# Optimization experiments

Hardware: AMD Instinct MI355X
Metric: run time of the kernel (lower is better)

## Reference

```python
import jax, jax.numpy as jnp
import numpy as np

N_DRUG = 20000
N_PROT = 30000
N = N_DRUG + N_PROT
F_DRUG = 128
F_PROT = 256
H = 64          # hidden_channels
OUT = 1         # out_channels
E = 1_600_000
L = 200_000
LAYERS = 3


def _lin_init(key, fan_in, fan_out):
    return jax.random.normal(key, (fan_in, fan_out), jnp.float32) / np.sqrt(fan_in)


def setup_inputs() -> dict:
    key = jax.random.key(0)
    ks = jax.random.split(key, 10)
    x_drug = jax.random.normal(ks[0], (N_DRUG, F_DRUG), jnp.float32)
    x_protein = jax.random.normal(ks[1], (N_PROT, F_PROT), jnp.float32)
    edge_index = jax.random.randint(ks[2], (2, E), 0, N, dtype=jnp.int64)
    edge_label_src = jax.random.randint(ks[3], (L,), 0, N_DRUG, dtype=jnp.int64)
    # protein label indices point into the concatenated [drug; protein] tensor
    edge_label_dst = jax.random.randint(ks[4], (L,), 0, N_PROT, dtype=jnp.int64) + N_DRUG
    W_drug = _lin_init(ks[5], F_DRUG, H)
    b_drug = jnp.zeros((H,), jnp.float32)
    W_prot = _lin_init(ks[6], F_PROT, H)
    b_prot = jnp.zeros((H,), jnp.float32)
    conv_W = jax.random.normal(ks[7], (LAYERS, H, H), jnp.float32) / np.sqrt(H)
    conv_b = jnp.zeros((LAYERS, H), jnp.float32)
    lin_W = _lin_init(ks[8], H, OUT)
    lin_b = jnp.zeros((OUT,), jnp.float32)
    return {
        "x_drug": x_drug, "x_protein": x_protein,
        "W_drug": W_drug, "b_drug": b_drug,
        "W_prot": W_prot, "b_prot": b_prot,
        "conv_W": conv_W, "conv_b": conv_b,
        "lin_W": lin_W, "lin_b": lin_b,
        "edge_index": edge_index,
        "edge_label_src": edge_label_src,
        "edge_label_dst": edge_label_dst,
    }


def reference(x_drug, x_protein, W_drug, b_drug, W_prot, b_prot,
              conv_W, conv_b, lin_W, lin_b,
              edge_index, edge_label_src, edge_label_dst):
    # type-specific input projections + relu
    hd = jax.nn.relu(x_drug @ W_drug + b_drug)
    hp = jax.nn.relu(x_protein @ W_prot + b_prot)
    x = jnp.concatenate([hd, hp], axis=0)  # [N, H]

    src, dst = edge_index[0], edge_index[1]
    # GCN normalization with self-loops: deg counts in-edges (by dst) + 1
    deg = jax.ops.segment_sum(jnp.ones_like(src, dtype=x.dtype), dst, num_segments=N) + 1.0
    dis = jax.lax.rsqrt(deg)               # deg >= 1 always
    edge_norm = (dis[src] * dis[dst])[:, None]   # [E, 1]
    self_norm = (dis * dis)[:, None]             # [N, 1]

    for l in range(LAYERS):
        xw = x @ conv_W[l]                                   # [N, H] dense GEMM
        agg = jax.ops.segment_sum(xw[src] * edge_norm, dst, num_segments=N)
        x = jax.nn.relu(agg + xw * self_norm + conv_b[l])

    # edge scoring head: gather endpoints, linear to 1, multiply, sigmoid
    sd = (x[edge_label_src] @ lin_W + lin_b)[:, 0]  # [L]
    sp = (x[edge_label_dst] @ lin_W + lin_b)[:, 0]  # [L]
    return jax.nn.sigmoid(sd * sp)
```

## Files before the change

kernel.cpp:

```cpp
#include <hip/hip_runtime.h>
#include <hip/hip_fp16.h>
#include <math.h>

#define N_DRUG 20000
#define N_PROT 30000
#define NN (N_DRUG + N_PROT)
#define F_DRUG 128
#define F_PROT 256
#define H 64
#define NE 1600000
#define NL 200000

#define NB_PROJD ((N_DRUG + 127) / 128)
#define NB_PROJP ((N_PROT + 127) / 128)
#define NB_CONV  ((NN + 255) / 256)
#define NB_ROW4  ((NN + 3) / 4)
#define NBK1 256
#define CH   ((NE + NBK1 - 1) / NBK1)
#define NB_BKT ((NN + 255) / 256)

typedef _Float16 h8 __attribute__((ext_vector_type(8)));
typedef _Float16 h4 __attribute__((ext_vector_type(4)));
typedef float f32x4 __attribute__((ext_vector_type(4)));

#define MFMA16(a, b, c) __builtin_amdgcn_mfma_f32_16x16x32_f16((a), (b), (c), 0, 0, 0)

__global__ __launch_bounds__(256) void k_wprep(
    const float* __restrict__ Wd, const float* __restrict__ Wp,
    const float* __restrict__ cw,
    _Float16* __restrict__ wdt, _Float16* __restrict__ wpt,
    _Float16* __restrict__ cwt) {
    int i = blockIdx.x * 256 + threadIdx.x;
    if (i < 64 * F_DRUG) {
        int c = i / F_DRUG, k = i % F_DRUG;
        wdt[i] = (_Float16)Wd[k * H + c];
    }
    if (i < 64 * F_PROT) {
        int c = i / F_PROT, k = i % F_PROT;
        wpt[i] = (_Float16)Wp[k * H + c];
    }
    if (i < 3 * 64 * 64) {
        int l = i >> 12, r = i & 4095;
        int c = r >> 6, k = r & 63;
        cwt[i] = (_Float16)cw[(l << 12) + k * H + c];
    }
}

template <int F>
__device__ __forceinline__ void proj_direct(
    const float* __restrict__ X, const _Float16* __restrict__ Wt,
    const float* __restrict__ bias, __half* __restrict__ out,
    int rows, int row_off, int bid) {
    int l = threadIdx.x & 63, wvi = threadIdx.x >> 6;
    int lr = l & 15, lq = l >> 4;
    int r0 = bid * 128 + wvi * 32;
    f32x4 acc[2][4];
    #pragma unroll
    for (int rt = 0; rt < 2; ++rt)
        #pragma unroll
        for (int n = 0; n < 4; ++n) acc[rt][n] = (f32x4){0.f, 0.f, 0.f, 0.f};

    for (int k0 = 0; k0 < F; k0 += 64) {
        h8 af[4][2];
        #pragma unroll
        for (int n = 0; n < 4; ++n)
            #pragma unroll
            for (int kk = 0; kk < 2; ++kk)
                af[n][kk] = *(const h8*)&Wt[(size_t)(n * 16 + lr) * F + k0 + kk * 32 + lq * 8];
        #pragma unroll
        for (int rt = 0; rt < 2; ++rt) {
            int r = r0 + rt * 16 + lr;
            int rc = (r < rows) ? r : (rows - 1);
            h8 bf[2];
            #pragma unroll
            for (int kk = 0; kk < 2; ++kk) {
                const float* xp = X + (size_t)rc * F + k0 + kk * 32 + lq * 8;
                float4 a = *(const float4*)xp;
                float4 b = *(const float4*)(xp + 4);
                h8 t;
                t[0] = (_Float16)a.x; t[1] = (_Float16)a.y;
                t[2] = (_Float16)a.z; t[3] = (_Float16)a.w;
                t[4] = (_Float16)b.x; t[5] = (_Float16)b.y;
                t[6] = (_Float16)b.z; t[7] = (_Float16)b.w;
                bf[kk] = t;
            }
            #pragma unroll
            for (int n = 0; n < 4; ++n) {
                acc[rt][n] = MFMA16(af[n][0], bf[0], acc[rt][n]);
                acc[rt][n] = MFMA16(af[n][1], bf[1], acc[rt][n]);
            }
        }
    }
    #pragma unroll
    for (int rt = 0; rt < 2; ++rt) {
        int r = r0 + rt * 16 + lr;
        if (r < rows) {
            #pragma unroll
            for (int n = 0; n < 4; ++n) {
                int c = n * 16 + lq * 4;
                float4 bv = *(const float4*)&bias[c];
                h4 hv;
                hv[0] = (_Float16)fmaxf(acc[rt][n][0] + bv.x, 0.f);
                hv[1] = (_Float16)fmaxf(acc[rt][n][1] + bv.y, 0.f);
                hv[2] = (_Float16)fmaxf(acc[rt][n][2] + bv.z, 0.f);
                hv[3] = (_Float16)fmaxf(acc[rt][n][3] + bv.w, 0.f);
                *(h4*)((_Float16*)out + (size_t)(row_off + r) * H + c) = hv;
            }
        }
    }
}

__device__ __forceinline__ void conv_direct(
    const __half* __restrict__ xin, const _Float16* __restrict__ Wt,
    __half* __restrict__ xout, int bid) {
    int l = threadIdx.x & 63, wvi = threadIdx.x >> 6;
    int lr = l & 15, lq = l >> 4;
    const _Float16* xh = (const _Float16*)xin;
    h8 af[4][2];
    #pragma unroll
    for (int n = 0; n < 4; ++n)
        #pragma unroll
        for (int kk = 0; kk < 2; ++kk)
            af[n][kk] = *(const h8*)&Wt[(size_t)(n * 16 + lr) * 64 + kk * 32 + lq * 8];
    int r0 = bid * 256 + wvi * 64;
    #pragma unroll
    for (int rt = 0; rt < 4; ++rt) {
        int r = r0 + rt * 16 + lr;
        int rc = (r < NN) ? r : (NN - 1);
        h8 bf0 = *(const h8*)&xh[(size_t)rc * H + lq * 8];
        h8 bf1 = *(const h8*)&xh[(size_t)rc * H + 32 + lq * 8];
        f32x4 a[4];
        #pragma unroll
        for (int n = 0; n < 4; ++n) {
            a[n] = (f32x4){0.f, 0.f, 0.f, 0.f};
            a[n] = MFMA16(af[n][0], bf0, a[n]);
            a[n] = MFMA16(af[n][1], bf1, a[n]);
        }
        if (r < NN) {
            #pragma unroll
            for (int n = 0; n < 4; ++n) {
                int c = n * 16 + lq * 4;
                h4 hv;
                hv[0] = (_Float16)a[n][0]; hv[1] = (_Float16)a[n][1];
                hv[2] = (_Float16)a[n][2]; hv[3] = (_Float16)a[n][3];
                *(h4*)((_Float16*)xout + (size_t)r * H + c) = hv;
            }
        }
    }
}

__global__ __launch_bounds__(256) void k_front(
    const float* __restrict__ xd, const _Float16* __restrict__ wdt, const float* __restrict__ bd,
    const float* __restrict__ xp, const _Float16* __restrict__ wpt, const float* __restrict__ bp,
    const int* __restrict__ ei, unsigned* __restrict__ bhist, __half* __restrict__ xbuf) {
    __shared__ unsigned lh[256];
    int bid = blockIdx.x;
    if (bid < NB_PROJD) {
        proj_direct<F_DRUG>(xd, wdt, bd, xbuf, N_DRUG, 0, bid);
    } else if (bid < NB_PROJD + NB_PROJP) {
        proj_direct<F_PROT>(xp, wpt, bp, xbuf, N_PROT, N_DRUG, bid - NB_PROJD);
    } else {
        int blk = bid - NB_PROJD - NB_PROJP;
        int t = threadIdx.x;
        lh[t] = 0;
        __syncthreads();
        int eb = blk * CH, ee = min(NE, eb + CH);
        for (int e = eb + t; e < ee; e += 256)
            atomicAdd(&lh[((unsigned)ei[NE + e]) >> 8], 1u);
        __syncthreads();
        bhist[(size_t)t * NBK1 + blk] = lh[t];
    }
}

__global__ __launch_bounds__(256) void kA(const unsigned* __restrict__ bhist,
                                          unsigned* __restrict__ rsum) {
    __shared__ unsigned s[256];
    int j = blockIdx.x, t = threadIdx.x;
    s[t] = bhist[(size_t)j * NBK1 + t];
    __syncthreads();
    for (int off = 128; off; off >>= 1) {
        if (t < off) s[t] += s[t + off];
        __syncthreads();
    }
    if (t == 0) rsum[j] = s[0];
}

__global__ __launch_bounds__(256) void kB(const unsigned* __restrict__ rsum,
                                          unsigned* __restrict__ rbase) {
    __shared__ unsigned s[256];
    int t = threadIdx.x;
    unsigned c = rsum[t];
    s[t] = c;
    __syncthreads();
    for (int off = 1; off < 256; off <<= 1) {
        unsigned v = s[t]; unsigned u = (t >= off) ? s[t - off] : 0;
        __syncthreads(); s[t] = v + u; __syncthreads();
    }
    rbase[t] = s[t] - c;
    if (t == 255) rbase[256] = s[255];
}

__global__ __launch_bounds__(256) void kC(unsigned* __restrict__ bhist,
                                          const unsigned* __restrict__ rbase) {
    __shared__ unsigned s[256];
    int j = blockIdx.x, t = threadIdx.x;
    unsigned c = bhist[(size_t)j * NBK1 + t];
    s[t] = c;
    __syncthreads();
    for (int off = 1; off < 256; off <<= 1) {
        unsigned v = s[t]; unsigned u = (t >= off) ? s[t - off] : 0;
        __syncthreads(); s[t] = v + u; __syncthreads();
    }
    bhist[(size_t)j * NBK1 + t] = rbase[j] + s[t] - c;
}

__global__ __launch_bounds__(256) void k_part(
    const int* __restrict__ ei, const unsigned* __restrict__ base,
    unsigned* __restrict__ tmp) {
    __shared__ unsigned lcur[256];
    int bid = blockIdx.x;
    int c = ((bid & 7) << 5) | (bid >> 3);
    int t = threadIdx.x;
    lcur[t] = base[(size_t)t * NBK1 + c];
    __syncthreads();
    int eb = c * CH, ee = min(NE, eb + CH);
    for (int e = eb + t; e < ee; e += 256) {
        unsigned s = (unsigned)ei[e];
        unsigned d = (unsigned)ei[NE + e];
        unsigned pos = atomicAdd(&lcur[d >> 8], 1u);
        tmp[pos] = ((d & 255u) << 16) | s;
    }
}

__global__ __launch_bounds__(256) void k_csrconv(
    const unsigned* __restrict__ tmp, const unsigned* __restrict__ rbase,
    int* __restrict__ rp, float* __restrict__ dis, unsigned short* __restrict__ csr,
    const __half* __restrict__ xbuf, const _Float16* __restrict__ cwt,
    __half* __restrict__ xwh) {
    __shared__ unsigned lbin[256], lofs[256], lcur[256];
    int bid = blockIdx.x;
    if (bid >= NB_BKT) {
        conv_direct(xbuf, cwt, xwh, bid - NB_BKT);
        return;
    }
    int b = bid, t = threadIdx.x;
    unsigned nb0 = rbase[b], nb1 = rbase[b + 1];
    lbin[t] = 0;
    __syncthreads();
    for (unsigned i = nb0 + t; i < nb1; i += 256)
        atomicAdd(&lbin[tmp[i] >> 16], 1u);
    __syncthreads();
    unsigned c = lbin[t];
    lofs[t] = c;
    __syncthreads();
    for (int off = 1; off < 256; off <<= 1) {
        unsigned v = lofs[t]; unsigned u = (t >= off) ? lofs[t - off] : 0;
        __syncthreads(); lofs[t] = v + u; __syncthreads();
    }
    unsigned r = nb0 + lofs[t] - c;
    int node = b * 256 + t;
    if (node < NN) {
        rp[node] = (int)r;
        dis[node] = rsqrtf((float)c + 1.0f);
    }
    lcur[t] = r;
    __syncthreads();
    for (unsigned i = nb0 + t; i < nb1; i += 256) {
        unsigned rec = tmp[i];
        unsigned pos = atomicAdd(&lcur[rec >> 16], 1u);
        csr[pos] = (unsigned short)(rec & 0xffffu);
    }
    if (b == 0 && t == 0) rp[NN] = NE;
}

__global__ __launch_bounds__(256) void k_conv(
    const __half* __restrict__ X, const _Float16* __restrict__ Wt, __half* __restrict__ out) {
    conv_direct(X, Wt, out, blockIdx.x);
}

template <bool FIRST, bool LAST>
__global__ __launch_bounds__(256) void k_spmm(
    const int* __restrict__ rp, const unsigned short* __restrict__ csr,
    unsigned* __restrict__ pack, const float* __restrict__ dis,
    const __half* __restrict__ xw,
    const float* __restrict__ bias, __half* __restrict__ xout,
    const float* __restrict__ lw, const float* __restrict__ lb,
    float* __restrict__ y) {
    int lane = threadIdx.x & 63;
    int d = blockIdx.x * 4 + (threadIdx.x >> 6);
    if (d >= NN) return;
    int q = lane >> 4, g = lane & 15;
    int beg = rp[d], end = rp[d + 1];
    float dd = dis[d];
    const _Float16* xh = (const _Float16*)xw;
    float ax = 0.f, ay = 0.f, az = 0.f, aw = 0.f;

    int n = end - beg; if (n > 64) n = 64;
    unsigned rv = 0;
    if (lane < n) {
        if (FIRST) {
            int s = csr[beg + lane];
            float w0 = dis[s] * dd;
            rv = (unsigned)s | ((unsigned)__half_as_ushort(__float2half(w0)) << 16);
            pack[beg + lane] = rv;
        } else rv = pack[beg + lane];
    }
    for (int b0 = beg; b0 < end; ) {
        int nb = b0 + 64;
        int n2 = end - nb; if (n2 > 64) n2 = 64;
        unsigned rv2 = 0;
        if (n2 > 0 && lane < n2) {
            if (FIRST) {
                int s = csr[nb + lane];
                float w0 = dis[s] * dd;
                rv2 = (unsigned)s | ((unsigned)__half_as_ushort(__float2half(w0)) << 16);
                pack[nb + lane] = rv2;
            } else rv2 = pack[nb + lane];
        }
        int nsteps = (n + 3) >> 2;
        for (int j0 = 0; j0 < nsteps; j0 += 8) {
            int m = nsteps - j0; if (m > 8) m = 8;
            h4 xv[8]; float wv[8];
            #pragma unroll
            for (int k = 0; k < 8; ++k) {
                if (k < m) {
                    unsigned r = __shfl(rv, (j0 + k) * 4 + q);
                    wv[k] = __half2float(__ushort_as_half((unsigned short)(r >> 16)));
                    xv[k] = *(const h4*)&xh[((r & 0xffffu) << 6) + (g << 2)];
                }
            }
            #pragma unroll
            for (int k = 0; k < 8; ++k) {
                if (k < m) {
                    ax += wv[k] * (float)xv[k][0];
                    ay += wv[k] * (float)xv[k][1];
                    az += wv[k] * (float)xv[k][2];
                    aw += wv[k] * (float)xv[k][3];
                }
            }
        }
        b0 = nb; n = n2; rv = rv2;
    }
    ax += __shfl_xor(ax, 16); ay += __shfl_xor(ay, 16);
    az += __shfl_xor(az, 16); aw += __shfl_xor(aw, 16);
    ax += __shfl_xor(ax, 32); ay += __shfl_xor(ay, 32);
    az += __shfl_xor(az, 32); aw += __shfl_xor(aw, 32);

    float sn = dd * dd;
    h4 xs = *(const h4*)&xh[((unsigned)d << 6) + (g << 2)];
    float4 bv = *(const float4*)&bias[g << 2];
    float vx = fmaxf(ax + sn * (float)xs[0] + bv.x, 0.f);
    float vy = fmaxf(ay + sn * (float)xs[1] + bv.y, 0.f);
    float vz = fmaxf(az + sn * (float)xs[2] + bv.z, 0.f);
    float vw = fmaxf(aw + sn * (float)xs[3] + bv.w, 0.f);
    if (LAST) {
        float4 lv = *(const float4*)&lw[g << 2];
        float t = vx * lv.x + vy * lv.y + vz * lv.z + vw * lv.w;
        #pragma unroll
        for (int off = 8; off; off >>= 1) t += __shfl_xor(t, off);
        if (lane == 0) y[d] = t + lb[0];
    } else if (q == 0) {
        h4 hv;
        hv[0] = (_Float16)vx; hv[1] = (_Float16)vy;
        hv[2] = (_Float16)vz; hv[3] = (_Float16)vw;
        *(h4*)((_Float16*)xout + ((size_t)d << 6) + (g << 2)) = hv;
    }
}

__global__ void k_out(const float* __restrict__ y, const int* __restrict__ ls,
                      const int* __restrict__ ld, float* __restrict__ out) {
    int e = blockIdx.x * blockDim.x + threadIdx.x;
    if (e < NL) {
        float z = y[ls[e]] * y[ld[e]];
        out[e] = 1.f / (1.f + __expf(-z));
    }
}

static inline size_t up256(size_t x) { return (x + 255) & ~(size_t)255; }

extern "C" void kernel_launch(void* const* d_in, const int* in_sizes, int n_in,
                              void* d_out, int out_size, void* d_ws, size_t ws_size,
                              hipStream_t stream) {
    const float* x_drug = (const float*)d_in[0];
    const float* x_prot = (const float*)d_in[1];
    const float* W_drug = (const float*)d_in[2];
    const float* b_drug = (const float*)d_in[3];
    const float* W_prot = (const float*)d_in[4];
    const float* b_prot = (const float*)d_in[5];
    const float* conv_W = (const float*)d_in[6];
    const float* conv_b = (const float*)d_in[7];
    const float* lin_W  = (const float*)d_in[8];
    const float* lin_b  = (const float*)d_in[9];
    const int*   ei     = (const int*)d_in[10];
    const int*   lsrc   = (const int*)d_in[11];
    const int*   ldst   = (const int*)d_in[12];
    float* out = (float*)d_out;

    char* w = (char*)d_ws;
    size_t off = 0;
    unsigned* bhist = (unsigned*)(w + off); off = up256(off + (size_t)256 * NBK1 * 4);
    unsigned* rsum  = (unsigned*)(w + off); off = up256(off + 256 * 4);
    unsigned* rbase = (unsigned*)(w + off); off = up256(off + 257 * 4);
    unsigned* tmp   = (unsigned*)(w + off); off = up256(off + (size_t)NE * 4);
    unsigned short* csr = (unsigned short*)(w + off); off = up256(off + (size_t)NE * 2);
    unsigned* pack  = (unsigned*)(w + off); off = up256(off + (size_t)NE * 4);
    int*    rp   = (int*)(w + off);    off = up256(off + (size_t)(NN + 1) * 4);
    float*  dis  = (float*)(w + off);  off = up256(off + (size_t)NN * 4);
    __half* xbuf = (__half*)(w + off); off = up256(off + (size_t)NN * H * 2);
    __half* xwh  = (__half*)(w + off); off = up256(off + (size_t)NN * H * 2);
    float*  y    = (float*)(w + off);  off = up256(off + (size_t)NN * 4);
    _Float16* wdt = (_Float16*)(w + off); off = up256(off + (size_t)64 * F_DRUG * 2);
    _Float16* wpt = (_Float16*)(w + off); off = up256(off + (size_t)64 * F_PROT * 2);
    _Float16* cwt = (_Float16*)(w + off); off = up256(off + (size_t)3 * 64 * 64 * 2);

    k_wprep<<<64, 256, 0, stream>>>(W_drug, W_prot, conv_W, wdt, wpt, cwt);

    k_front<<<NB_PROJD + NB_PROJP + NBK1, 256, 0, stream>>>(
        x_drug, wdt, b_drug, x_prot, wpt, b_prot, ei, bhist, xbuf);

    kA<<<256, 256, 0, stream>>>(bhist, rsum);
    kB<<<1, 256, 0, stream>>>(rsum, rbase);
    kC<<<256, 256, 0, stream>>>(bhist, rbase);

    k_part<<<NBK1, 256, 0, stream>>>(ei, bhist, tmp);

    k_csrconv<<<NB_BKT + NB_CONV, 256, 0, stream>>>(
        tmp, rbase, rp, dis, csr, xbuf, cwt, xwh);

    k_spmm<true, false><<<NB_ROW4, 256, 0, stream>>>(
        rp, csr, pack, dis, xwh, conv_b, xbuf, nullptr, nullptr, nullptr);
    k_conv<<<NB_CONV, 256, 0, stream>>>(xbuf, cwt + 4096, xwh);
    k_spmm<false, false><<<NB_ROW4, 256, 0, stream>>>(
        rp, csr, pack, dis, xwh, conv_b + H, xbuf, nullptr, nullptr, nullptr);
    k_conv<<<NB_CONV, 256, 0, stream>>>(xbuf, cwt + 8192, xwh);
    k_spmm<false, true><<<NB_ROW4, 256, 0, stream>>>(
        rp, csr, pack, dis, xwh, conv_b + 2 * H, nullptr, lin_W, lin_b, y);

    k_out<<<(NL + 255) / 256, 256, 0, stream>>>(y, lsrc, ldst, out);
}
```

Measured before the change: 206.2 us.

## Split hidden features into two 32-wide halves and run SpMM per half

Stores activations as two separate 32-column fp16 planes and runs each sparse aggregation twice, once per half, so each gathered row is 64 bytes and each pass's working set is half as large for better cache hit rates. The pack array is reread with nontemporal loads in the later passes. It doubles the SpMM launches and the CSR/pack traversal. The final linear head is split into two partial sums that the output kernel adds together.

```diff
diff --git a/kernel.cpp b/kernel.cpp
--- a/kernel.cpp
+++ b/kernel.cpp
@@ -49,7 +49,8 @@
 template <int F>
 __device__ __forceinline__ void proj_direct(
     const float* __restrict__ X, const _Float16* __restrict__ Wt,
-    const float* __restrict__ bias, __half* __restrict__ out,
+    const float* __restrict__ bias,
+    _Float16* __restrict__ xlo, _Float16* __restrict__ xhi,
     int rows, int row_off, int bid) {
     int l = threadIdx.x & 63, wvi = threadIdx.x >> 6;
     int lr = l & 15, lq = l >> 4;
@@ -104,18 +105,21 @@
                 hv[1] = (_Float16)fmaxf(acc[rt][n][1] + bv.y, 0.f);
                 hv[2] = (_Float16)fmaxf(acc[rt][n][2] + bv.z, 0.f);
                 hv[3] = (_Float16)fmaxf(acc[rt][n][3] + bv.w, 0.f);
-                *(h4*)((_Float16*)out + (size_t)(row_off + r) * H + c) = hv;
+                _Float16* dst = (n < 2)
+                    ? (xlo + (size_t)(row_off + r) * 32 + c)
+                    : (xhi + (size_t)(row_off + r) * 32 + (c - 32));
+                *(h4*)dst = hv;
             }
         }
     }
 }
 
 __device__ __forceinline__ void conv_direct(
-    const __half* __restrict__ xin, const _Float16* __restrict__ Wt,
-    __half* __restrict__ xout, int bid) {
+    const _Float16* __restrict__ xlo, const _Float16* __restrict__ xhi,
+    const _Float16* __restrict__ Wt,
+    _Float16* __restrict__ olo, _Float16* __restrict__ ohi, int bid) {
     int l = threadIdx.x & 63, wvi = threadIdx.x >> 6;
     int lr = l & 15, lq = l >> 4;
-    const _Float16* xh = (const _Float16*)xin;
     h8 af[4][2];
     #pragma unroll
     for (int n = 0; n < 4; ++n)
@@ -127,8 +131,8 @@
     for (int rt = 0; rt < 4; ++rt) {
         int r = r0 + rt * 16 + lr;
         int rc = (r < NN) ? r : (NN - 1);
-        h8 bf0 = *(const h8*)&xh[(size_t)rc * H + lq * 8];
-        h8 bf1 = *(const h8*)&xh[(size_t)rc * H + 32 + lq * 8];
+        h8 bf0 = *(const h8*)&xlo[(size_t)rc * 32 + lq * 8];
+        h8 bf1 = *(const h8*)&xhi[(size_t)rc * 32 + lq * 8];
         f32x4 a[4];
         #pragma unroll
         for (int n = 0; n < 4; ++n) {
@@ -143,7 +147,10 @@
                 h4 hv;
                 hv[0] = (_Float16)a[n][0]; hv[1] = (_Float16)a[n][1];
                 hv[2] = (_Float16)a[n][2]; hv[3] = (_Float16)a[n][3];
-                *(h4*)((_Float16*)xout + (size_t)r * H + c) = hv;
+                _Float16* dst = (n < 2)
+                    ? (olo + (size_t)r * 32 + c)
+                    : (ohi + (size_t)r * 32 + (c - 32));
+                *(h4*)dst = hv;
             }
         }
     }
@@ -152,13 +159,14 @@
 __global__ __launch_bounds__(256) void k_front(
     const float* __restrict__ xd, const _Float16* __restrict__ wdt, const float* __restrict__ bd,
     const float* __restrict__ xp, const _Float16* __restrict__ wpt, const float* __restrict__ bp,
-    const int* __restrict__ ei, unsigned* __restrict__ bhist, __half* __restrict__ xbuf) {
+    const int* __restrict__ ei, unsigned* __restrict__ bhist,
+    _Float16* __restrict__ xlo, _Float16* __restrict__ xhi) {
     __shared__ unsigned lh[256];
     int bid = blockIdx.x;
     if (bid < NB_PROJD) {
-        proj_direct<F_DRUG>(xd, wdt, bd, xbuf, N_DRUG, 0, bid);
+        proj_direct<F_DRUG>(xd, wdt, bd, xlo, xhi, N_DRUG, 0, bid);
     } else if (bid < NB_PROJD + NB_PROJP) {
-        proj_direct<F_PROT>(xp, wpt, bp, xbuf, N_PROT, N_DRUG, bid - NB_PROJD);
+        proj_direct<F_PROT>(xp, wpt, bp, xlo, xhi, N_PROT, N_DRUG, bid - NB_PROJD);
     } else {
         int blk = bid - NB_PROJD - NB_PROJP;
         int t = threadIdx.x;
@@ -235,12 +243,13 @@
 __global__ __launch_bounds__(256) void k_csrconv(
     const unsigned* __restrict__ tmp, const unsigned* __restrict__ rbase,
     int* __restrict__ rp, float* __restrict__ dis, unsigned short* __restrict__ csr,
-    const __half* __restrict__ xbuf, const _Float16* __restrict__ cwt,
-    __half* __restrict__ xwh) {
+    const _Float16* __restrict__ xlo, const _Float16* __restrict__ xhi,
+    const _Float16* __restrict__ cwt,
+    _Float16* __restrict__ olo, _Float16* __restrict__ ohi) {
     __shared__ unsigned lbin[256], lofs[256], lcur[256];
     int bid = blockIdx.x;
     if (bid >= NB_BKT) {
-        conv_direct(xbuf, cwt, xwh, bid - NB_BKT);
+        conv_direct(xlo, xhi, cwt, olo, ohi, bid - NB_BKT);
         return;
     }
     int b = bid, t = threadIdx.x;
@@ -274,25 +283,25 @@
 }
 
 __global__ __launch_bounds__(256) void k_conv(
-    const __half* __restrict__ X, const _Float16* __restrict__ Wt, __half* __restrict__ out) {
-    conv_direct(X, Wt, out, blockIdx.x);
+    const _Float16* __restrict__ xlo, const _Float16* __restrict__ xhi,
+    const _Float16* __restrict__ Wt,
+    _Float16* __restrict__ olo, _Float16* __restrict__ ohi) {
+    conv_direct(xlo, xhi, Wt, olo, ohi, blockIdx.x);
 }
 
 template <bool FIRST, bool LAST>
-__global__ __launch_bounds__(256) void k_spmm(
+__global__ __launch_bounds__(256) void k_spmm2(
     const int* __restrict__ rp, const unsigned short* __restrict__ csr,
     unsigned* __restrict__ pack, const float* __restrict__ dis,
-    const __half* __restrict__ xw,
-    const float* __restrict__ bias, __half* __restrict__ xout,
-    const float* __restrict__ lw, const float* __restrict__ lb,
-    float* __restrict__ y) {
+    const _Float16* __restrict__ xws ,
+    const float* __restrict__ bias32, _Float16* __restrict__ xouts ,
+    const float* __restrict__ lw32, float* __restrict__ ypart) {
     int lane = threadIdx.x & 63;
     int d = blockIdx.x * 4 + (threadIdx.x >> 6);
     if (d >= NN) return;
-    int q = lane >> 4, g = lane & 15;
+    int q = lane >> 3, g = lane & 7;
     int beg = rp[d], end = rp[d + 1];
     float dd = dis[d];
-    const _Float16* xh = (const _Float16*)xw;
     float ax = 0.f, ay = 0.f, az = 0.f, aw = 0.f;
 
     int n = end - beg; if (n > 64) n = 64;
@@ -303,7 +312,7 @@
             float w0 = dis[s] * dd;
             rv = (unsigned)s | ((unsigned)__half_as_ushort(__float2half(w0)) << 16);
             pack[beg + lane] = rv;
-        } else rv = pack[beg + lane];
+        } else rv = __builtin_nontemporal_load(&pack[beg + lane]);
     }
     for (int b0 = beg; b0 < end; ) {
         int nb = b0 + 64;
@@ -315,22 +324,22 @@
                 float w0 = dis[s] * dd;
                 rv2 = (unsigned)s | ((unsigned)__half_as_ushort(__float2half(w0)) << 16);
                 pack[nb + lane] = rv2;
-            } else rv2 = pack[nb + lane];
-        }
-        int nsteps = (n + 3) >> 2;
-        for (int j0 = 0; j0 < nsteps; j0 += 8) {
-            int m = nsteps - j0; if (m > 8) m = 8;
-            h4 xv[8]; float wv[8];
-            #pragma unroll
-            for (int k = 0; k < 8; ++k) {
+            } else rv2 = __builtin_nontemporal_load(&pack[nb + lane]);
+        }
+        int nsteps = (n + 7) >> 3;
+        for (int j0 = 0; j0 < nsteps; j0 += 4) {
+            int m = nsteps - j0; if (m > 4) m = 4;
+            h4 xv[4]; float wv[4];
+            #pragma unroll
+            for (int k = 0; k < 4; ++k) {
                 if (k < m) {
-                    unsigned r = __shfl(rv, (j0 + k) * 4 + q);
+                    unsigned r = __shfl(rv, (j0 + k) * 8 + q);
                     wv[k] = __half2float(__ushort_as_half((unsigned short)(r >> 16)));
-                    xv[k] = *(const h4*)&xh[((r & 0xffffu) << 6) + (g << 2)];
+                    xv[k] = *(const h4*)&xws[((r & 0xffffu) << 5) + (g << 2)];
                 }
             }
             #pragma unroll
-            for (int k = 0; k < 8; ++k) {
+            for (int k = 0; k < 4; ++k) {
                 if (k < m) {
                     ax += wv[k] * (float)xv[k][0];
                     ay += wv[k] * (float)xv[k][1];
@@ -341,37 +350,43 @@
         }
         b0 = nb; n = n2; rv = rv2;
     }
-    ax += __shfl_xor(ax, 16); ay += __shfl_xor(ay, 16);
-    az += __shfl_xor(az, 16); aw += __shfl_xor(aw, 16);
-    ax += __shfl_xor(ax, 32); ay += __shfl_xor(ay, 32);
-    az += __shfl_xor(az, 32); aw += __shfl_xor(aw, 32);
+    #pragma unroll
+    for (int off = 8; off < 64; off <<= 1) {
+        ax += __shfl_xor(ax, off); ay += __shfl_xor(ay, off);
+        az += __shfl_xor(az, off); aw += __shfl_xor(aw, off);
+    }
 
     float sn = dd * dd;
-    h4 xs = *(const h4*)&xh[((unsigned)d << 6) + (g << 2)];
-    float4 bv = *(const float4*)&bias[g << 2];
+    h4 xs = *(const h4*)&xws[((unsigned)d << 5) + (g << 2)];
+    float4 bv = *(const float4*)&bias32[g << 2];
     float vx = fmaxf(ax + sn * (float)xs[0] + bv.x, 0.f);
     float vy = fmaxf(ay + sn * (float)xs[1] + bv.y, 0.f);
     float vz = fmaxf(az + sn * (float)xs[2] + bv.z, 0.f);
     float vw = fmaxf(aw + sn * (float)xs[3] + bv.w, 0.f);
     if (LAST) {
-        float4 lv = *(const float4*)&lw[g << 2];
+        float4 lv = *(const float4*)&lw32[g << 2];
         float t = vx * lv.x + vy * lv.y + vz * lv.z + vw * lv.w;
-        #pragma unroll
-        for (int off = 8; off; off >>= 1) t += __shfl_xor(t, off);
-        if (lane == 0) y[d] = t + lb[0];
+        t += __shfl_xor(t, 1); t += __shfl_xor(t, 2); t += __shfl_xor(t, 4);
+        if (lane == 0) ypart[d] = t;
     } else if (q == 0) {
         h4 hv;
         hv[0] = (_Float16)vx; hv[1] = (_Float16)vy;
         hv[2] = (_Float16)vz; hv[3] = (_Float16)vw;
-        *(h4*)((_Float16*)xout + ((size_t)d << 6) + (g << 2)) = hv;
-    }
-}
-
-__global__ void k_out(const float* __restrict__ y, const int* __restrict__ ls,
-                      const int* __restrict__ ld, float* __restrict__ out) {
+        *(h4*)(xouts + ((size_t)d << 5) + (g << 2)) = hv;
+    }
+}
+
+__global__ void k_out(const float* __restrict__ ylo, const float* __restrict__ yhi,
+                      const float* __restrict__ lb,
+                      const int* __restrict__ ls, const int* __restrict__ ld,
+                      float* __restrict__ out) {
     int e = blockIdx.x * blockDim.x + threadIdx.x;
     if (e < NL) {
-        float z = y[ls[e]] * y[ld[e]];
+        float b = lb[0];
+        int s = ls[e], t = ld[e];
+        float sd = ylo[s] + yhi[s] + b;
+        float sp = ylo[t] + yhi[t] + b;
+        float z = sd * sp;
         out[e] = 1.f / (1.f + __expf(-z));
     }
 }
@@ -406,9 +421,12 @@
     unsigned* pack  = (unsigned*)(w + off); off = up256(off + (size_t)NE * 4);
     int*    rp   = (int*)(w + off);    off = up256(off + (size_t)(NN + 1) * 4);
     float*  dis  = (float*)(w + off);  off = up256(off + (size_t)NN * 4);
-    __half* xbuf = (__half*)(w + off); off = up256(off + (size_t)NN * H * 2);
-    __half* xwh  = (__half*)(w + off); off = up256(off + (size_t)NN * H * 2);
-    float*  y    = (float*)(w + off);  off = up256(off + (size_t)NN * 4);
+    _Float16* xblo = (_Float16*)(w + off); off = up256(off + (size_t)NN * 32 * 2);
+    _Float16* xbhi = (_Float16*)(w + off); off = up256(off + (size_t)NN * 32 * 2);
+    _Float16* xwlo = (_Float16*)(w + off); off = up256(off + (size_t)NN * 32 * 2);
+    _Float16* xwhi = (_Float16*)(w + off); off = up256(off + (size_t)NN * 32 * 2);
+    float*  ylo  = (float*)(w + off);  off = up256(off + (size_t)NN * 4);
+    float*  yhi  = (float*)(w + off);  off = up256(off + (size_t)NN * 4);
     _Float16* wdt = (_Float16*)(w + off); off = up256(off + (size_t)64 * F_DRUG * 2);
     _Float16* wpt = (_Float16*)(w + off); off = up256(off + (size_t)64 * F_PROT * 2);
     _Float16* cwt = (_Float16*)(w + off); off = up256(off + (size_t)3 * 64 * 64 * 2);
@@ -416,7 +434,7 @@
     k_wprep<<<64, 256, 0, stream>>>(W_drug, W_prot, conv_W, wdt, wpt, cwt);
 
     k_front<<<NB_PROJD + NB_PROJP + NBK1, 256, 0, stream>>>(
-        x_drug, wdt, b_drug, x_prot, wpt, b_prot, ei, bhist, xbuf);
+        x_drug, wdt, b_drug, x_prot, wpt, b_prot, ei, bhist, xblo, xbhi);
 
     kA<<<256, 256, 0, stream>>>(bhist, rsum);
     kB<<<1, 256, 0, stream>>>(rsum, rbase);
@@ -425,16 +443,22 @@
     k_part<<<NBK1, 256, 0, stream>>>(ei, bhist, tmp);
 
     k_csrconv<<<NB_BKT + NB_CONV, 256, 0, stream>>>(
-        tmp, rbase, rp, dis, csr, xbuf, cwt, xwh);
-
-    k_spmm<true, false><<<NB_ROW4, 256, 0, stream>>>(
-        rp, csr, pack, dis, xwh, conv_b, xbuf, nullptr, nullptr, nullptr);
-    k_conv<<<NB_CONV, 256, 0, stream>>>(xbuf, cwt + 4096, xwh);
-    k_spmm<false, false><<<NB_ROW4, 256, 0, stream>>>(
-        rp, csr, pack, dis, xwh, conv_b + H, xbuf, nullptr, nullptr, nullptr);
-    k_conv<<<NB_CONV, 256, 0, stream>>>(xbuf, cwt + 8192, xwh);
-    k_spmm<false, true><<<NB_ROW4, 256, 0, stream>>>(
-        rp, csr, pack, dis, xwh, conv_b + 2 * H, nullptr, lin_W, lin_b, y);
-
-    k_out<<<(NL + 255) / 256, 256, 0, stream>>>(y, lsrc, ldst, out);
-}
+        tmp, rbase, rp, dis, csr, xblo, xbhi, cwt, xwlo, xwhi);
+
+    k_spmm2<true, false><<<NB_ROW4, 256, 0, stream>>>(
+        rp, csr, pack, dis, xwlo, conv_b, xblo, nullptr, nullptr);
+    k_spmm2<false, false><<<NB_ROW4, 256, 0, stream>>>(
+        rp, csr, pack, dis, xwhi, conv_b + 32, xbhi, nullptr, nullptr);
+    k_conv<<<NB_CONV, 256, 0, stream>>>(xblo, xbhi, cwt + 4096, xwlo, xwhi);
+    k_spmm2<false, false><<<NB_ROW4, 256, 0, stream>>>(
+        rp, csr, pack, dis, xwlo, conv_b + 64, xblo, nullptr, nullptr);
+    k_spmm2<false, false><<<NB_ROW4, 256, 0, stream>>>(
+        rp, csr, pack, dis, xwhi, conv_b + 96, xbhi, nullptr, nullptr);
+    k_conv<<<NB_CONV, 256, 0, stream>>>(xblo, xbhi, cwt + 8192, xwlo, xwhi);
+    k_spmm2<false, true><<<NB_ROW4, 256, 0, stream>>>(
+        rp, csr, pack, dis, xwlo, conv_b + 128, nullptr, lin_W, ylo);
+    k_spmm2<false, true><<<NB_ROW4, 256, 0, stream>>>(
+        rp, csr, pack, dis, xwhi, conv_b + 160, nullptr, lin_W + 32, yhi);
+
+    k_out<<<(NL + 255) / 256, 256, 0, stream>>>(ylo, yhi, lin_b, lsrc, ldst, out);
+}
```

Measured after the change: 251.3 us. +21.9%, slower.
